# Performance work log

Measured on AMD Instinct MI355X. Metric: run time of the kernel, lower is better.

The kernel has to match this reference:

```python
import jax, jax.numpy as jnp
import numpy as np

N_USERS = 100000
N_ITEMS = 50000
N_NODES = N_USERS + N_ITEMS
DIM = 64
N_EDGES = 1200000
BATCH = 4096


def _propagate(edge_index, emb):
    # row = source, col = destination (out[dst] += norm * emb[src])
    row, col = edge_index[0], edge_index[1]
    n = emb.shape[0]
    # degree counted over row occurrences only (faithful to `degree(row, ...)`)
    deg = jax.ops.segment_sum(jnp.ones_like(row, dtype=emb.dtype), row, num_segments=n)
    dinv = jnp.where(deg > 0, deg ** -0.5, 0.0).astype(emb.dtype)
    norm = dinv[row] * dinv[col]  # [E]
    msgs = norm[:, None] * emb[row]  # [E, D] gather + scale
    return jax.ops.segment_sum(msgs, col, num_segments=n)  # scatter-add into dst


def setup_inputs() -> dict:
    key = jax.random.key(0)
    ks = jax.random.split(key, 10)
    xavier = (6.0 / (N_USERS + DIM)) ** 0.5  # approximate xavier bounds per table
    user_emb = jax.random.uniform(ks[0], (N_USERS, DIM), jnp.float32, -xavier, xavier)
    xavier_i = (6.0 / (N_ITEMS + DIM)) ** 0.5
    item_emb = jax.random.uniform(ks[1], (N_ITEMS, DIM), jnp.float32, -xavier_i, xavier_i)
    lim = (1.0 / DIM) ** 0.5
    W1 = jax.random.uniform(ks[2], (DIM, DIM), jnp.float32, -lim, lim)
    b1 = jax.random.uniform(ks[3], (DIM,), jnp.float32, -lim, lim)
    W2 = jax.random.uniform(ks[4], (DIM, DIM), jnp.float32, -lim, lim)
    b2 = jax.random.uniform(ks[5], (DIM,), jnp.float32, -lim, lim)
    users = jax.random.randint(ks[6], (BATCH,), 0, N_USERS)
    items = jax.random.randint(ks[7], (BATCH,), 0, N_ITEMS)
    edge_index = jax.random.randint(ks[8], (2, N_EDGES), 0, N_NODES)
    return {"users": users, "items": items, "edge_index": edge_index,
            "user_emb": user_emb, "item_emb": item_emb,
            "W1": W1, "b1": b1, "W2": W2, "b2": b2}


def reference(users, items, edge_index, user_emb, item_emb, W1, b1, W2, b2):
    all_emb = jnp.concatenate([user_emb, item_emb], axis=0)  # [N, D]
    # layer 0: propagate -> linear -> relu
    all_emb = _propagate(edge_index, all_emb)
    all_emb = jax.nn.relu(all_emb @ W1.T + b1)
    # layer 1 (last): propagate -> linear (no relu)
    all_emb = _propagate(edge_index, all_emb)
    all_emb = all_emb @ W2.T + b2
    user_final = all_emb[:N_USERS]
    item_final = all_emb[N_USERS:]
    scores = jnp.sum(user_final[users] * item_final[items], axis=1)  # [B]
    return scores
```

## Files before the change

kernel.cpp:

```cpp
#include <hip/hip_runtime.h>
#include <math.h>

constexpr int NU = 100000;
constexpr int NI = 50000;
constexpr int NN = 150000;
constexpr int D  = 64;
constexpr int NE = 1200000;
constexpr int NE4 = NE / 4;
constexpr int B  = 4096;
constexpr int CAPB = 64;
constexpr int CAP2 = 40;

constexpr int NCHUNK = 3;
constexpr int CHUNK  = 65536;
constexpr int CWORDS = CHUNK / 4;
constexpr int WORDS  = 37504;
constexpr int RWORDS = 37500;
constexpr int NSLICE = 80;
constexpr int SLICE4 = NE4 / NSLICE;

constexpr int BMW = 4704;
constexpr int CZ4 = 150016 / 4;


__global__ void __launch_bounds__(1024) k_flag(const int* __restrict__ users,
                                               const int* __restrict__ items,
                                               unsigned int* __restrict__ bm0,
                                               int* __restrict__ bidx,
                                               int* __restrict__ nb,
                                               unsigned int* __restrict__ bm1,
                                               int* __restrict__ cntBd,
                                               int* __restrict__ ncnt) {
    for (int i = threadIdx.x; i < BMW; i += 1024) bm1[i] = 0;
    for (int i = threadIdx.x; i < 8448; i += 1024) cntBd[i] = 0;
    if (threadIdx.x == 0) *ncnt = 0;

    __shared__ unsigned int sbm[BMW];
    __shared__ int snb;
    for (int i = threadIdx.x; i < BMW; i += 1024) sbm[i] = 0;
    if (threadIdx.x == 0) snb = 0;
    __syncthreads();
    for (int t = threadIdx.x; t < 2 * B; t += 1024) {
        const int node = (t < B) ? users[t] : items[t - B] + NU;
        const unsigned int old = atomicOr(&sbm[node >> 5], 1u << (node & 31));
        if (!((old >> (node & 31)) & 1)) bidx[node] = atomicAdd(&snb, 1);
    }
    __syncthreads();
    for (int i = threadIdx.x; i < BMW; i += 1024) bm0[i] = sbm[i];
    if (threadIdx.x == 0) *nb = snb;
}

__global__ void __launch_bounds__(256) k_hist(const int* __restrict__ row,
                                              unsigned int* __restrict__ hcopy,
                                              int4* __restrict__ cnt2dz) {
    for (int i = blockIdx.x * 256 + threadIdx.x; i < CZ4; i += gridDim.x * 256)
        cnt2dz[i] = make_int4(0, 0, 0, 0);

    __shared__ unsigned int lh[CWORDS];
    const int ci = blockIdx.x / NSLICE;
    const int si = blockIdx.x % NSLICE;
    const int lo = ci * CHUNK;
    const int cw = (ci == NCHUNK - 1) ? (WORDS - (NCHUNK - 1) * CWORDS) : CWORDS;
    for (int w = threadIdx.x; w < cw; w += 256) lh[w] = 0;
    __syncthreads();
    const int4* r4 = reinterpret_cast<const int4*>(row) + (size_t)si * SLICE4;
    const unsigned int span = (unsigned)(cw * 4);
    for (int t = threadIdx.x; t < SLICE4; t += 256) {
        const int4 r = r4[t];
        int v;
        v = r.x - lo; if ((unsigned)v < span) atomicAdd(&lh[v >> 2], 1u << (8 * (v & 3)));
        v = r.y - lo; if ((unsigned)v < span) atomicAdd(&lh[v >> 2], 1u << (8 * (v & 3)));
        v = r.z - lo; if ((unsigned)v < span) atomicAdd(&lh[v >> 2], 1u << (8 * (v & 3)));
        v = r.w - lo; if ((unsigned)v < span) atomicAdd(&lh[v >> 2], 1u << (8 * (v & 3)));
    }
    __syncthreads();
    unsigned int* dst = hcopy + (size_t)si * WORDS + ci * CWORDS;
    for (int w = threadIdx.x; w < cw; w += 256) dst[w] = lh[w];
}

__global__ void k_mark(const int* __restrict__ row, const int* __restrict__ col,
                       const unsigned int* __restrict__ bm0,
                       const int* __restrict__ bidx,
                       int* __restrict__ cntBd, int* __restrict__ csrBd,
                       unsigned int* __restrict__ bm1) {
    const int t = blockIdx.x * blockDim.x + threadIdx.x;
    if (t >= NE4) return;
    const int4 r = reinterpret_cast<const int4*>(row)[t];
    const int4 c = reinterpret_cast<const int4*>(col)[t];
    #define E1(rr, cc) if ((bm0[(cc) >> 5] >> ((cc) & 31)) & 1) { \
        const int bi = bidx[cc]; \
        const int s = atomicAdd(&cntBd[bi], 1); \
        csrBd[bi * CAPB + s] = rr; \
        atomicOr(&bm1[(rr) >> 5], 1u << ((rr) & 31)); }
    E1(r.x, c.x) E1(r.y, c.y) E1(r.z, c.z) E1(r.w, c.w)
    #undef E1
}

__global__ void __launch_bounds__(256) k_pass2d(const int* __restrict__ row,
                                                const int* __restrict__ col,
                                                const unsigned int* __restrict__ bm1,
                                                int* __restrict__ cnt2d,
                                                int* __restrict__ csr2d,
                                                const unsigned int* __restrict__ hcopy,
                                                float* __restrict__ dinv,
                                                int* __restrict__ list,
                                                int* __restrict__ ncnt) {
    if (blockIdx.x < 147) {
        const int w = blockIdx.x * 256 + threadIdx.x;
        if (w >= RWORDS) return;
        unsigned int s = 0;
        #pragma unroll 8
        for (int si = 0; si < NSLICE; ++si) s += hcopy[(size_t)si * WORDS + w];
        const int d0 = s & 255, d1 = (s >> 8) & 255, d2 = (s >> 16) & 255, d3 = (int)(s >> 24);
        float4 dv;
        dv.x = d0 > 0 ? 1.0f / sqrtf((float)d0) : 0.0f;
        dv.y = d1 > 0 ? 1.0f / sqrtf((float)d1) : 0.0f;
        dv.z = d2 > 0 ? 1.0f / sqrtf((float)d2) : 0.0f;
        dv.w = d3 > 0 ? 1.0f / sqrtf((float)d3) : 0.0f;
        reinterpret_cast<float4*>(dinv)[w] = dv;
        const unsigned int bits = (bm1[w >> 3] >> ((w & 7) * 4)) & 0xFu;
        const int n0 = w * 4;
        if (bits & 1u) list[atomicAdd(ncnt, 1)] = n0;
        if (bits & 2u) list[atomicAdd(ncnt, 1)] = n0 + 1;
        if (bits & 4u) list[atomicAdd(ncnt, 1)] = n0 + 2;
        if (bits & 8u) list[atomicAdd(ncnt, 1)] = n0 + 3;
    } else {
        const int t = (blockIdx.x - 147) * 256 + threadIdx.x;
        if (t >= NE4) return;
        const int4 r = reinterpret_cast<const int4*>(row)[t];
        const int4 c = reinterpret_cast<const int4*>(col)[t];
        #define E2(rr, cc) if ((bm1[(cc) >> 5] >> ((cc) & 31)) & 1) { \
            const int s = atomicAdd(&cnt2d[cc], 1); \
            csr2d[cc * CAP2 + s] = rr; }
        E2(r.x, c.x) E2(r.y, c.y) E2(r.z, c.z) E2(r.w, c.w)
        #undef E2
    }
}

__global__ void k_gather1(const int* __restrict__ list, const int* __restrict__ ncnt,
                          const int* __restrict__ cnt2d, const int* __restrict__ csr2d,
                          const float* __restrict__ dinv,
                          const float* __restrict__ embU, const float* __restrict__ embI,
                          float* __restrict__ out) {
    const int lane = threadIdx.x & 63;
    const int n = *ncnt;
    const int nwv = gridDim.x * (blockDim.x >> 6);
    for (int idx = blockIdx.x * (blockDim.x >> 6) + (threadIdx.x >> 6);
         idx < n; idx += nwv) {
        const int c = list[idx];
        const int ne = cnt2d[c];
        const int* es = csr2d + (size_t)c * CAP2;
        float a0 = 0.0f, a1 = 0.0f, a2 = 0.0f, a3 = 0.0f;
        int e = 0;
        for (; e + 3 < ne; e += 4) {
            const int4 r = *reinterpret_cast<const int4*>(es + e);
            const float d0 = dinv[r.x], d1 = dinv[r.y], d2 = dinv[r.z], d3 = dinv[r.w];
            const float* s0 = (r.x < NU) ? embU + (size_t)r.x * D : embI + (size_t)(r.x - NU) * D;
            const float* s1 = (r.y < NU) ? embU + (size_t)r.y * D : embI + (size_t)(r.y - NU) * D;
            const float* s2 = (r.z < NU) ? embU + (size_t)r.z * D : embI + (size_t)(r.z - NU) * D;
            const float* s3 = (r.w < NU) ? embU + (size_t)r.w * D : embI + (size_t)(r.w - NU) * D;
            a0 = fmaf(d0, s0[lane], a0);
            a1 = fmaf(d1, s1[lane], a1);
            a2 = fmaf(d2, s2[lane], a2);
            a3 = fmaf(d3, s3[lane], a3);
        }
        for (; e < ne; ++e) {
            const int r = es[e];
            const float* s = (r < NU) ? embU + (size_t)r * D : embI + (size_t)(r - NU) * D;
            a0 = fmaf(dinv[r], s[lane], a0);
        }
        out[(size_t)c * D + lane] = dinv[c] * ((a0 + a1) + (a2 + a3));
    }
}

__global__ void __launch_bounds__(256) k_mlp_relu(const int* __restrict__ list,
                                                  const int* __restrict__ ncnt,
                                                  float* __restrict__ emb,
                                                  const float* __restrict__ W,
                                                  const float* __restrict__ b) {
    const int lane = threadIdx.x & 63;
    float w[D];
    #pragma unroll
    for (int k4 = 0; k4 < D / 4; ++k4) {
        const float4 v = *reinterpret_cast<const float4*>(W + (size_t)lane * D + k4 * 4);
        w[k4 * 4 + 0] = v.x; w[k4 * 4 + 1] = v.y;
        w[k4 * 4 + 2] = v.z; w[k4 * 4 + 3] = v.w;
    }
    const float bias = b[lane];

    const int n = *ncnt;
    const int wid = blockIdx.x * (blockDim.x >> 6) + (threadIdx.x >> 6);
    const int nw  = gridDim.x * (blockDim.x >> 6);
    for (int i4 = wid * 4; i4 < n; i4 += nw * 4) {
        const int r0 = list[i4];
        const int r1 = (i4 + 1 < n) ? list[i4 + 1] : r0;
        const int r2 = (i4 + 2 < n) ? list[i4 + 2] : r0;
        const int r3 = (i4 + 3 < n) ? list[i4 + 3] : r0;
        float* x0 = emb + (size_t)r0 * D;
        float* x1 = emb + (size_t)r1 * D;
        float* x2 = emb + (size_t)r2 * D;
        float* x3 = emb + (size_t)r3 * D;
        const float xv0 = x0[lane], xv1 = x1[lane], xv2 = x2[lane], xv3 = x3[lane];
        float a0 = bias, a1 = bias, a2 = bias, a3 = bias;
        #pragma unroll
        for (int k = 0; k < D; ++k) {
            const float wk = w[k];
            a0 = fmaf(__int_as_float(__builtin_amdgcn_readlane(__float_as_int(xv0), k)), wk, a0);
            a1 = fmaf(__int_as_float(__builtin_amdgcn_readlane(__float_as_int(xv1), k)), wk, a1);
            a2 = fmaf(__int_as_float(__builtin_amdgcn_readlane(__float_as_int(xv2), k)), wk, a2);
            a3 = fmaf(__int_as_float(__builtin_amdgcn_readlane(__float_as_int(xv3), k)), wk, a3);
        }
        x0[lane] = fmaxf(a0, 0.0f);
        x1[lane] = fmaxf(a1, 0.0f);
        x2[lane] = fmaxf(a2, 0.0f);
        x3[lane] = fmaxf(a3, 0.0f);
    }
}

__global__ void __launch_bounds__(256) k_score2(const int* __restrict__ users,
                                                const int* __restrict__ items,
                                                const int* __restrict__ bidx,
                                                const int* __restrict__ cntBd,
                                                const int* __restrict__ csrBd,
                                                const float* __restrict__ dinv,
                                                const float* __restrict__ embA,
                                                const float* __restrict__ W,
                                                const float* __restrict__ b,
                                                float* __restrict__ out) {
    __shared__ float sy[2][2][D];
    const int lane = threadIdx.x & 63;
    const int wid  = threadIdx.x >> 6;
    const int pp   = wid >> 1;
    const int t    = wid & 1;
    const int p    = blockIdx.x * 2 + pp;

    float w[D];
    #pragma unroll
    for (int k4 = 0; k4 < D / 4; ++k4) {
        const float4 v = *reinterpret_cast<const float4*>(W + (size_t)lane * D + k4 * 4);
        w[k4 * 4 + 0] = v.x; w[k4 * 4 + 1] = v.y;
        w[k4 * 4 + 2] = v.z; w[k4 * 4 + 3] = v.w;
    }

    const int c  = (t == 0) ? users[p] : items[p] + NU;
    const int bi = bidx[c];
    const int n  = cntBd[bi];
    const int* es = csrBd + (size_t)bi * CAPB;
    float a0 = 0.0f, a1 = 0.0f, a2 = 0.0f, a3 = 0.0f;
    int e = 0;
    for (; e + 3 < n; e += 4) {
        const int4 r = *reinterpret_cast<const int4*>(es + e);
        a0 = fmaf(dinv[r.x], embA[(size_t)r.x * D + lane], a0);
        a1 = fmaf(dinv[r.y], embA[(size_t)r.y * D + lane], a1);
        a2 = fmaf(dinv[r.z], embA[(size_t)r.z * D + lane], a2);
        a3 = fmaf(dinv[r.w], embA[(size_t)r.w * D + lane], a3);
    }
    for (; e < n; ++e) {
        const int r = es[e];
        a0 = fmaf(dinv[r], embA[(size_t)r * D + lane], a0);
    }
    const float x = dinv[c] * ((a0 + a1) + (a2 + a3));

    float y = b[lane];
    #pragma unroll
    for (int k = 0; k < D; ++k)
        y = fmaf(__int_as_float(__builtin_amdgcn_readlane(__float_as_int(x), k)),
                 w[k], y);
    sy[pp][t][lane] = y;
    __syncthreads();
    if (t == 0) {
        float prod = sy[pp][0][lane] * sy[pp][1][lane];
        #pragma unroll
        for (int off = 32; off >= 1; off >>= 1) prod += __shfl_down(prod, off, 64);
        if (lane == 0) out[p] = prod;
    }
}

extern "C" void kernel_launch(void* const* d_in, const int* in_sizes, int n_in,
                              void* d_out, int out_size, void* d_ws, size_t ws_size,
                              hipStream_t stream) {
    const int*   users    = (const int*)d_in[0];
    const int*   items    = (const int*)d_in[1];
    const int*   edge     = (const int*)d_in[2];
    const float* user_emb = (const float*)d_in[3];
    const float* item_emb = (const float*)d_in[4];
    const float* W1       = (const float*)d_in[5];
    const float* b1       = (const float*)d_in[6];
    const float* W2       = (const float*)d_in[7];
    const float* b2       = (const float*)d_in[8];
    float*       out      = (float*)d_out;

    const int* row  = edge;
    const int* colp = edge + NE;

    unsigned int* bm1   = (unsigned int*)d_ws;
    int*   cnt2d = (int*)d_ws + 4704;
    int*   cntBd = (int*)d_ws + 154720;
    int*   ncnt  = (int*)d_ws + 163168;
    unsigned int* bm0   = (unsigned int*)d_ws + 163184;
    int*   nb    = (int*)d_ws + 167888;
    float* dinv  = (float*)d_ws + 167904;
    int*   bidx  = (int*)d_ws + 317920;
    int*   list  = (int*)d_ws + 467936;
    int*   csrBd = (int*)d_ws + 617952;
    int*   csr2d = (int*)d_ws + 1158624;
    float* embA  = (float*)d_ws + 7159264;
    unsigned int* hcopy = (unsigned int*)embA;

    k_flag <<<1, 1024, 0, stream>>>(users, items, bm0, bidx, nb, bm1, cntBd, ncnt);
    k_hist <<<NCHUNK * NSLICE, 256, 0, stream>>>(row, hcopy, (int4*)cnt2d);
    k_mark <<<(NE4 + 255) / 256, 256, 0, stream>>>(row, colp, bm0, bidx, cntBd, csrBd, bm1);
    k_pass2d<<<147 + (NE4 + 255) / 256, 256, 0, stream>>>(row, colp, bm1, cnt2d, csr2d,
                                                          hcopy, dinv, list, ncnt);
    k_gather1 <<<8192, 256, 0, stream>>>(list, ncnt, cnt2d, csr2d, dinv,
                                         user_emb, item_emb, embA);
    k_mlp_relu<<<2048, 256, 0, stream>>>(list, ncnt, embA, W1, b1);
    k_score2<<<B / 2, 256, 0, stream>>>(users, items, bidx, cntBd, csrBd, dinv, embA,
                                        W2, b2, out);
}
```

Measured before the change: 157.8 us.

## Build second-hop CSR via column histograms and prefix offsets instead of global atomics

The restricted CSR for second-hop destinations was built with per-edge global atomicAdd on cnt2d. It is now built by computing per-slice destination histograms in LDS alongside the row degree histogram, prefix-summing them per slice to get base offsets, and scattering edges with LDS atomics plus those bases. This replaces contended global atomics with shared-memory atomics and also makes slot order deterministic. The cost is an extra full pass over the col array, more histogram blocks, and larger workspace traffic for hcopy2 and base_pk.

After: 192.7 us. 1.22x slower.

```diff
diff --git a/kernel.cpp b/kernel.cpp
--- a/kernel.cpp
+++ b/kernel.cpp
@@ -18,9 +18,13 @@
 constexpr int RWORDS = 37500;
 constexpr int NSLICE = 80;
 constexpr int SLICE4 = NE4 / NSLICE;
+constexpr int NHB    = NCHUNK * NSLICE;
+
+constexpr int CH2    = 6;
+constexpr int CW2    = 6272;
+constexpr int CHUNK2 = CW2 * 4;
 
 constexpr int BMW = 4704;
-constexpr int CZ4 = 150016 / 4;
 
 
 __global__ void __launch_bounds__(1024) k_flag(const int* __restrict__ users,
@@ -50,20 +54,23 @@
     if (threadIdx.x == 0) *nb = snb;
 }
 
-__global__ void __launch_bounds__(256) k_hist(const int* __restrict__ row,
-                                              unsigned int* __restrict__ hcopy,
-                                              int4* __restrict__ cnt2dz) {
-    for (int i = blockIdx.x * 256 + threadIdx.x; i < CZ4; i += gridDim.x * 256)
-        cnt2dz[i] = make_int4(0, 0, 0, 0);
+__global__ void __launch_bounds__(256) k_hist2(const int* __restrict__ row,
+                                               const int* __restrict__ col,
+                                               unsigned int* __restrict__ hcopy,
+                                               unsigned int* __restrict__ hcopy2) {
+    const bool isCol = (blockIdx.x >= NHB);
+    const int  bid   = isCol ? (blockIdx.x - NHB) : blockIdx.x;
+    const int* src   = isCol ? col : row;
+    unsigned int* dstbase = isCol ? hcopy2 : hcopy;
 
     __shared__ unsigned int lh[CWORDS];
-    const int ci = blockIdx.x / NSLICE;
-    const int si = blockIdx.x % NSLICE;
+    const int ci = bid / NSLICE;
+    const int si = bid % NSLICE;
     const int lo = ci * CHUNK;
     const int cw = (ci == NCHUNK - 1) ? (WORDS - (NCHUNK - 1) * CWORDS) : CWORDS;
     for (int w = threadIdx.x; w < cw; w += 256) lh[w] = 0;
     __syncthreads();
-    const int4* r4 = reinterpret_cast<const int4*>(row) + (size_t)si * SLICE4;
+    const int4* r4 = reinterpret_cast<const int4*>(src) + (size_t)si * SLICE4;
     const unsigned int span = (unsigned)(cw * 4);
     for (int t = threadIdx.x; t < SLICE4; t += 256) {
         const int4 r = r4[t];
@@ -74,7 +81,7 @@
         v = r.w - lo; if ((unsigned)v < span) atomicAdd(&lh[v >> 2], 1u << (8 * (v & 3)));
     }
     __syncthreads();
-    unsigned int* dst = hcopy + (size_t)si * WORDS + ci * CWORDS;
+    unsigned int* dst = dstbase + (size_t)si * WORDS + ci * CWORDS;
     for (int w = threadIdx.x; w < cw; w += 256) dst[w] = lh[w];
 }
 
@@ -96,44 +103,68 @@
     #undef E1
 }
 
-__global__ void __launch_bounds__(256) k_pass2d(const int* __restrict__ row,
-                                                const int* __restrict__ col,
-                                                const unsigned int* __restrict__ bm1,
-                                                int* __restrict__ cnt2d,
-                                                int* __restrict__ csr2d,
-                                                const unsigned int* __restrict__ hcopy,
-                                                float* __restrict__ dinv,
-                                                int* __restrict__ list,
-                                                int* __restrict__ ncnt) {
-    if (blockIdx.x < 147) {
-        const int w = blockIdx.x * 256 + threadIdx.x;
-        if (w >= RWORDS) return;
-        unsigned int s = 0;
-        #pragma unroll 8
-        for (int si = 0; si < NSLICE; ++si) s += hcopy[(size_t)si * WORDS + w];
-        const int d0 = s & 255, d1 = (s >> 8) & 255, d2 = (s >> 16) & 255, d3 = (int)(s >> 24);
-        float4 dv;
-        dv.x = d0 > 0 ? 1.0f / sqrtf((float)d0) : 0.0f;
-        dv.y = d1 > 0 ? 1.0f / sqrtf((float)d1) : 0.0f;
-        dv.z = d2 > 0 ? 1.0f / sqrtf((float)d2) : 0.0f;
-        dv.w = d3 > 0 ? 1.0f / sqrtf((float)d3) : 0.0f;
-        reinterpret_cast<float4*>(dinv)[w] = dv;
-        const unsigned int bits = (bm1[w >> 3] >> ((w & 7) * 4)) & 0xFu;
-        const int n0 = w * 4;
-        if (bits & 1u) list[atomicAdd(ncnt, 1)] = n0;
-        if (bits & 2u) list[atomicAdd(ncnt, 1)] = n0 + 1;
-        if (bits & 4u) list[atomicAdd(ncnt, 1)] = n0 + 2;
-        if (bits & 8u) list[atomicAdd(ncnt, 1)] = n0 + 3;
-    } else {
-        const int t = (blockIdx.x - 147) * 256 + threadIdx.x;
-        if (t >= NE4) return;
-        const int4 r = reinterpret_cast<const int4*>(row)[t];
-        const int4 c = reinterpret_cast<const int4*>(col)[t];
-        #define E2(rr, cc) if ((bm1[(cc) >> 5] >> ((cc) & 31)) & 1) { \
-            const int s = atomicAdd(&cnt2d[cc], 1); \
-            csr2d[cc * CAP2 + s] = rr; }
-        E2(r.x, c.x) E2(r.y, c.y) E2(r.z, c.z) E2(r.w, c.w)
-        #undef E2
+__global__ void k_dinvc2(const unsigned int* __restrict__ hcopy,
+                         const unsigned int* __restrict__ hcopy2,
+                         float* __restrict__ dinv, int* __restrict__ cnt2d,
+                         unsigned int* __restrict__ base_pk,
+                         const unsigned int* __restrict__ bm1,
+                         int* __restrict__ list, int* __restrict__ ncnt) {
+    const int w = blockIdx.x * blockDim.x + threadIdx.x;
+    if (w >= RWORDS) return;
+    unsigned int s = 0;
+    #pragma unroll 8
+    for (int si = 0; si < NSLICE; ++si) s += hcopy[(size_t)si * WORDS + w];
+    const int d0 = s & 255, d1 = (s >> 8) & 255, d2 = (s >> 16) & 255, d3 = (int)(s >> 24);
+    float4 dv;
+    dv.x = d0 > 0 ? 1.0f / sqrtf((float)d0) : 0.0f;
+    dv.y = d1 > 0 ? 1.0f / sqrtf((float)d1) : 0.0f;
+    dv.z = d2 > 0 ? 1.0f / sqrtf((float)d2) : 0.0f;
+    dv.w = d3 > 0 ? 1.0f / sqrtf((float)d3) : 0.0f;
+    reinterpret_cast<float4*>(dinv)[w] = dv;
+    unsigned int run = 0;
+    #pragma unroll 8
+    for (int si = 0; si < NSLICE; ++si) {
+        base_pk[(size_t)si * WORDS + w] = run;
+        run += hcopy2[(size_t)si * WORDS + w];
+    }
+    int4 ct;
+    ct.x = run & 255; ct.y = (run >> 8) & 255; ct.z = (run >> 16) & 255; ct.w = (int)(run >> 24);
+    reinterpret_cast<int4*>(cnt2d)[w] = ct;
+    const unsigned int bits = (bm1[w >> 3] >> ((w & 7) * 4)) & 0xFu;
+    const int n0 = w * 4;
+    if (bits & 1u) list[atomicAdd(ncnt, 1)] = n0;
+    if (bits & 2u) list[atomicAdd(ncnt, 1)] = n0 + 1;
+    if (bits & 4u) list[atomicAdd(ncnt, 1)] = n0 + 2;
+    if (bits & 8u) list[atomicAdd(ncnt, 1)] = n0 + 3;
+}
+
+__global__ void __launch_bounds__(256) k_scatter(const int* __restrict__ row,
+                                                 const int* __restrict__ col,
+                                                 const unsigned int* __restrict__ bm1,
+                                                 const unsigned int* __restrict__ base_pk,
+                                                 int* __restrict__ csr2d) {
+    __shared__ unsigned int lcur[CW2];
+    const int ci = blockIdx.x / NSLICE;
+    const int si = blockIdx.x % NSLICE;
+    const int lo = ci * CHUNK2;
+    const int cw = (ci == CH2 - 1) ? (WORDS - (CH2 - 1) * CW2) : CW2;
+    for (int i = threadIdx.x; i < cw; i += 256) lcur[i] = 0;
+    __syncthreads();
+    const int4* r4 = reinterpret_cast<const int4*>(row) + (size_t)si * SLICE4;
+    const int4* c4 = reinterpret_cast<const int4*>(col) + (size_t)si * SLICE4;
+    const unsigned int span = (unsigned)(cw * 4);
+    const unsigned int* bpk = base_pk + (size_t)si * WORDS;
+    for (int t = threadIdx.x; t < SLICE4; t += 256) {
+        const int4 r = r4[t];
+        const int4 c = c4[t];
+        #define E3(rr, cc) { const int v = (cc) - lo; \
+            if ((unsigned)v < span && ((bm1[(cc) >> 5] >> ((cc) & 31)) & 1)) { \
+                const unsigned int old = atomicAdd(&lcur[v >> 2], 1u << (8 * (v & 3))); \
+                const int oldb = (old >> (8 * (v & 3))) & 255; \
+                const int slot = (int)((bpk[(cc) >> 2] >> (8 * ((cc) & 3))) & 255) + oldb; \
+                csr2d[(cc) * CAP2 + slot] = rr; } }
+        E3(r.x, c.x) E3(r.y, c.y) E3(r.z, c.z) E3(r.w, c.w)
+        #undef E3
     }
 }
 
@@ -305,13 +336,16 @@
     int*   csrBd = (int*)d_ws + 617952;
     int*   csr2d = (int*)d_ws + 1158624;
     float* embA  = (float*)d_ws + 7159264;
-    unsigned int* hcopy = (unsigned int*)embA;
+    unsigned int* hcopy   = (unsigned int*)embA;
+    unsigned int* hcopy2  = (unsigned int*)embA + 3000320;
+    unsigned int* base_pk = (unsigned int*)embA + 6000640;
 
     k_flag <<<1, 1024, 0, stream>>>(users, items, bm0, bidx, nb, bm1, cntBd, ncnt);
-    k_hist <<<NCHUNK * NSLICE, 256, 0, stream>>>(row, hcopy, (int4*)cnt2d);
+    k_hist2<<<2 * NHB, 256, 0, stream>>>(row, colp, hcopy, hcopy2);
     k_mark <<<(NE4 + 255) / 256, 256, 0, stream>>>(row, colp, bm0, bidx, cntBd, csrBd, bm1);
-    k_pass2d<<<147 + (NE4 + 255) / 256, 256, 0, stream>>>(row, colp, bm1, cnt2d, csr2d,
-                                                          hcopy, dinv, list, ncnt);
+    k_dinvc2<<<(RWORDS + 255) / 256, 256, 0, stream>>>(hcopy, hcopy2, dinv, cnt2d,
+                                                       base_pk, bm1, list, ncnt);
+    k_scatter<<<CH2 * NSLICE, 256, 0, stream>>>(row, colp, bm1, base_pk, csr2d);
     k_gather1 <<<8192, 256, 0, stream>>>(list, ncnt, cnt2d, csr2d, dinv,
                                          user_emb, item_emb, embA);
     k_mlp_relu<<<2048, 256, 0, stream>>>(list, ncnt, embA, W1, b1);
```
